# Kernel tuning notes

Measured on AMD Instinct MI355X. Metric: run time of the kernel, lower is better.

Reference implementation:

```python
import jax, jax.numpy as jnp
import numpy as np

B, N = 2048, 4095  # batch, number of spherical points (cumsum length = N+1)


def setup_inputs() -> dict:
    key = jax.random.key(0)
    k1, k2, k3, k4, k5 = jax.random.split(key, 5)
    return {
        "origin_3D": jax.random.uniform(k1, (B, 3, 1), dtype=jnp.float32),
        "spherical_3D": jax.random.uniform(k2, (B, 3, N), dtype=jnp.float32),
        "origin_2D": jax.random.uniform(k3, (B, 3, 1), dtype=jnp.float32),
        "spherical_2D": jax.random.uniform(k4, (B, 3, N), dtype=jnp.float32),
        "deformation_field": jax.random.uniform(k5, (B, 2, N), dtype=jnp.float32),
    }


def _cart(origin, spherical):
    # spherical: [B, 3, N] with rows (r, theta, phi)
    r, theta, phi = spherical[:, 0, :], spherical[:, 1, :], spherical[:, 2, :]
    st = jnp.sin(theta)
    x = r * st * jnp.cos(phi)
    y = r * st * jnp.sin(phi)
    z = r * jnp.cos(theta)
    shape = jnp.stack((x, y, z), axis=1)            # [B, 3, N]
    full = jnp.concatenate((origin, shape), axis=2)  # [B, 3, N+1]
    # torch.matmul(full, triu(ones)) == prefix sum along the last axis
    return jnp.cumsum(full, axis=2)


def reference(origin_3D, spherical_3D, origin_2D, spherical_2D, deformation_field):
    spherical_3D_deformed = spherical_3D.at[:, 1:, :].add(deformation_field)
    original_cart = _cart(origin_2D, spherical_2D)            # [B, 3, N+1]
    deformed_cart = _cart(origin_3D, spherical_3D_deformed)   # [B, 3, N+1]
    per_pt = jnp.sum(jnp.abs(deformed_cart - original_cart), axis=1)  # [B, N+1]
    return jnp.sum(jnp.mean(per_pt, axis=1))  # scalar
```

## Files before the change

### kernel.cpp

```cpp
#include <hip/hip_runtime.h>


#define BATCH 2048
#define NPTS  4095
#define POS   4096
#define T     512
#define NW    8
#define M     8
#define CH    8
#define BUFSZ 4352

__launch_bounds__(T, 6)
__global__ void mpd_loss_kernel(const float* __restrict__ origin3,
                                const float* __restrict__ sph3,
                                const float* __restrict__ origin2,
                                const float* __restrict__ sph2,
                                const float* __restrict__ def,
                                float* __restrict__ bsum) {
    __shared__ float bufx[BUFSZ];
    __shared__ float bufy[BUFSZ];
    __shared__ float bufz[BUFSZ];
    __shared__ float wtotx[NW], wtoty[NW], wtotz[NW];
    __shared__ float wsum[NW];

    const int b    = blockIdx.x;
    const int t    = threadIdx.x;
    const int lane = t & 63;
    const int w    = t >> 6;

    const float* r3  = sph3 + (size_t)b * 3 * NPTS;
    const float* th3 = r3 + NPTS;
    const float* ph3 = th3 + NPTS;
    const float* r2  = sph2 + (size_t)b * 3 * NPTS;
    const float* th2 = r2 + NPTS;
    const float* ph2 = th2 + NPTS;
    const float* d0  = def + (size_t)b * 2 * NPTS;
    const float* d1  = d0 + NPTS;

    #pragma unroll
    for (int m = 0; m < M; ++m) {
        const int j = m * T + t;
        float dx, dy, dz;
        if (m == 0 && t == 0) {
            const float* o3 = origin3 + (size_t)b * 3;
            const float* o2 = origin2 + (size_t)b * 3;
            dx = o3[0] - o2[0];
            dy = o3[1] - o2[1];
            dz = o3[2] - o2[2];
        } else {
            const int n = j - 1;
            const float R3  = r3[n];
            const float Th3 = th3[n] + d0[n];
            const float Ph3 = ph3[n] + d1[n];
            const float R2  = r2[n];
            const float Th2 = th2[n];
            const float Ph2 = ph2[n];
            float s3, c3, sp3, cp3, s2, c2, sp2, cp2;
            __sincosf(Th3, &s3, &c3);
            __sincosf(Ph3, &sp3, &cp3);
            __sincosf(Th2, &s2, &c2);
            __sincosf(Ph2, &sp2, &cp2);
            const float rs3 = R3 * s3;
            const float rs2 = R2 * s2;
            dx = rs3 * cp3 - rs2 * cp2;
            dy = rs3 * sp3 - rs2 * sp2;
            dz = R3 * c3 - R2 * c2;
        }
        const int a = j + (j >> 4);
        bufx[a] = dx;
        bufy[a] = dy;
        bufz[a] = dz;
    }
    __syncthreads();

    const int jb = t * CH;
    const int ba = jb + (jb >> 4);
    float vx[CH], vy[CH], vz[CH];
    float tx = 0.f, ty = 0.f, tz = 0.f;
    #pragma unroll
    for (int k = 0; k < CH; ++k) {
        vx[k] = bufx[ba + k]; tx += vx[k];
        vy[k] = bufy[ba + k]; ty += vy[k];
        vz[k] = bufz[ba + k]; tz += vz[k];
    }

    float ix = tx, iy = ty, iz = tz;
    #pragma unroll
    for (int off = 1; off < 64; off <<= 1) {
        const float ux = __shfl_up(ix, off, 64);
        const float uy = __shfl_up(iy, off, 64);
        const float uz = __shfl_up(iz, off, 64);
        if (lane >= off) { ix += ux; iy += uy; iz += uz; }
    }
    if (lane == 63) { wtotx[w] = ix; wtoty[w] = iy; wtotz[w] = iz; }
    __syncthreads();

    float wox = 0.f, woy = 0.f, woz = 0.f;
    #pragma unroll
    for (int ww = 0; ww < NW; ++ww) {
        if (ww < w) { wox += wtotx[ww]; woy += wtoty[ww]; woz += wtotz[ww]; }
    }

    float px = wox + (ix - tx);
    float py = woy + (iy - ty);
    float pz = woz + (iz - tz);
    float acc = 0.f;
    #pragma unroll
    for (int k = 0; k < CH; ++k) {
        px += vx[k]; py += vy[k]; pz += vz[k];
        acc += fabsf(px) + fabsf(py) + fabsf(pz);
    }

    #pragma unroll
    for (int off = 32; off > 0; off >>= 1) acc += __shfl_down(acc, off, 64);
    if (lane == 0) wsum[w] = acc;
    __syncthreads();
    if (t == 0) {
        float s = 0.f;
        #pragma unroll
        for (int i = 0; i < NW; ++i) s += wsum[i];
        bsum[b] = s * (1.0f / POS);
    }
}

__launch_bounds__(256)
__global__ void reduce_kernel(const float* __restrict__ bsum, float* __restrict__ out) {
    const int t = threadIdx.x;
    float acc = 0.f;
    #pragma unroll
    for (int i = 0; i < BATCH / 256; ++i) acc += bsum[t + i * 256];
    #pragma unroll
    for (int off = 32; off > 0; off >>= 1) acc += __shfl_down(acc, off, 64);
    __shared__ float wred[4];
    if ((t & 63) == 0) wred[t >> 6] = acc;
    __syncthreads();
    if (t == 0) out[0] = wred[0] + wred[1] + wred[2] + wred[3];
}

extern "C" void kernel_launch(void* const* d_in, const int* in_sizes, int n_in,
                              void* d_out, int out_size, void* d_ws, size_t ws_size,
                              hipStream_t stream) {
    const float* origin3 = (const float*)d_in[0];
    const float* sph3    = (const float*)d_in[1];
    const float* origin2 = (const float*)d_in[2];
    const float* sph2    = (const float*)d_in[3];
    const float* def     = (const float*)d_in[4];
    float* out  = (float*)d_out;
    float* bsum = (float*)d_ws;

    mpd_loss_kernel<<<BATCH, T, 0, stream>>>(origin3, sph3, origin2, sph2, def, bsum);
    reduce_kernel<<<1, 256, 0, stream>>>(bsum, out);
}
```

Baseline: 267.7 us.

## Load contiguous points per thread with vector loads and drop the shared-memory transpose

Each thread now reads its own contiguous block of eight points straight from global memory as two 4-wide vector loads per input row, with the last thread shifting its second load to stay in bounds. It computes the Cartesian deltas in registers and feeds them directly into the scan, so the large shared staging buffers and one barrier go away. The origin term is added to every prefix instead of being stored as element zero. The loads are unaligned and strided by 32 bytes per thread, which may coalesce less well than the old lane-contiguous reads, and the occupancy hint drops from 6 to 4 blocks.

```diff
diff --git a/kernel.cpp b/kernel.cpp
--- a/kernel.cpp
+++ b/kernel.cpp
@@ -6,27 +6,25 @@
 #define POS   4096
 #define T     512
 #define NW    8
-#define M     8
 #define CH    8
-#define BUFSZ 4352
 
-__launch_bounds__(T, 6)
+typedef float f4 __attribute__((ext_vector_type(4), aligned(4)));
+
+__launch_bounds__(T, 4)
 __global__ void mpd_loss_kernel(const float* __restrict__ origin3,
                                 const float* __restrict__ sph3,
                                 const float* __restrict__ origin2,
                                 const float* __restrict__ sph2,
                                 const float* __restrict__ def,
                                 float* __restrict__ bsum) {
-    __shared__ float bufx[BUFSZ];
-    __shared__ float bufy[BUFSZ];
-    __shared__ float bufz[BUFSZ];
-    __shared__ float wtotx[NW], wtoty[NW], wtotz[NW];
+    __shared__ float wtot[3][NW];
     __shared__ float wsum[NW];
 
     const int b    = blockIdx.x;
     const int t    = threadIdx.x;
     const int lane = t & 63;
     const int w    = t >> 6;
+    const bool lastT = (t == T - 1);
 
     const float* r3  = sph3 + (size_t)b * 3 * NPTS;
     const float* th3 = r3 + NPTS;
@@ -37,51 +35,56 @@
     const float* d0  = def + (size_t)b * 2 * NPTS;
     const float* d1  = d0 + NPTS;
 
-    #pragma unroll
-    for (int m = 0; m < M; ++m) {
-        const int j = m * T + t;
-        float dx, dy, dz;
-        if (m == 0 && t == 0) {
-            const float* o3 = origin3 + (size_t)b * 3;
-            const float* o2 = origin2 + (size_t)b * 3;
-            dx = o3[0] - o2[0];
-            dy = o3[1] - o2[1];
-            dz = o3[2] - o2[2];
-        } else {
-            const int n = j - 1;
-            const float R3  = r3[n];
-            const float Th3 = th3[n] + d0[n];
-            const float Ph3 = ph3[n] + d1[n];
-            const float R2  = r2[n];
-            const float Th2 = th2[n];
-            const float Ph2 = ph2[n];
-            float s3, c3, sp3, cp3, s2, c2, sp2, cp2;
-            __sincosf(Th3, &s3, &c3);
-            __sincosf(Ph3, &sp3, &cp3);
-            __sincosf(Th2, &s2, &c2);
-            __sincosf(Ph2, &sp2, &cp2);
-            const float rs3 = R3 * s3;
-            const float rs2 = R2 * s2;
-            dx = rs3 * cp3 - rs2 * cp2;
-            dy = rs3 * sp3 - rs2 * sp2;
-            dz = R3 * c3 - R2 * c2;
-        }
-        const int a = j + (j >> 4);
-        bufx[a] = dx;
-        bufy[a] = dy;
-        bufz[a] = dz;
-    }
-    __syncthreads();
+    const int n0 = t * CH;
+    const int n1 = lastT ? (n0 + 3) : (n0 + 4);
 
-    const int jb = t * CH;
-    const int ba = jb + (jb >> 4);
-    float vx[CH], vy[CH], vz[CH];
+    const f4 aR3 = *(const f4*)(r3  + n0);  const f4 bR3 = *(const f4*)(r3  + n1);
+    const f4 aT3 = *(const f4*)(th3 + n0);  const f4 bT3 = *(const f4*)(th3 + n1);
+    const f4 aP3 = *(const f4*)(ph3 + n0);  const f4 bP3 = *(const f4*)(ph3 + n1);
+    const f4 aR2 = *(const f4*)(r2  + n0);  const f4 bR2 = *(const f4*)(r2  + n1);
+    const f4 aT2 = *(const f4*)(th2 + n0);  const f4 bT2 = *(const f4*)(th2 + n1);
+    const f4 aP2 = *(const f4*)(ph2 + n0);  const f4 bP2 = *(const f4*)(ph2 + n1);
+    const f4 aD0 = *(const f4*)(d0  + n0);  const f4 bD0 = *(const f4*)(d0  + n1);
+    const f4 aD1 = *(const f4*)(d1  + n0);  const f4 bD1 = *(const f4*)(d1  + n1);
+
+    #define EXT(A, Bv, out)                          \
+        out[0] = A[0]; out[1] = A[1];                \
+        out[2] = A[2]; out[3] = A[3];                \
+        out[4] = lastT ? Bv[1] : Bv[0];              \
+        out[5] = lastT ? Bv[2] : Bv[1];              \
+        out[6] = lastT ? Bv[3] : Bv[2];              \
+        out[7] = Bv[3];
+
+    float eR3[8], eT3[8], eP3[8], eR2[8], eT2[8], eP2[8], eD0[8], eD1[8];
+    EXT(aR3, bR3, eR3); EXT(aT3, bT3, eT3); EXT(aP3, bP3, eP3);
+    EXT(aR2, bR2, eR2); EXT(aT2, bT2, eT2); EXT(aP2, bP2, eP2);
+    EXT(aD0, bD0, eD0); EXT(aD1, bD1, eD1);
+    #undef EXT
+
+    float dx[CH], dy[CH], dz[CH];
     float tx = 0.f, ty = 0.f, tz = 0.f;
     #pragma unroll
     for (int k = 0; k < CH; ++k) {
-        vx[k] = bufx[ba + k]; tx += vx[k];
-        vy[k] = bufy[ba + k]; ty += vy[k];
-        vz[k] = bufz[ba + k]; tz += vz[k];
+        const bool valid = (k < 7) || !lastT;
+        const float R3  = eR3[k];
+        const float Th3 = eT3[k] + eD0[k];
+        const float Ph3 = eP3[k] + eD1[k];
+        const float R2  = eR2[k];
+        const float Th2 = eT2[k];
+        const float Ph2 = eP2[k];
+        float s3, c3, sp3, cp3, s2, c2, sp2, cp2;
+        __sincosf(Th3, &s3, &c3);
+        __sincosf(Ph3, &sp3, &cp3);
+        __sincosf(Th2, &s2, &c2);
+        __sincosf(Ph2, &sp2, &cp2);
+        const float rs3 = R3 * s3;
+        const float rs2 = R2 * s2;
+        float ddx = rs3 * cp3 - rs2 * cp2;
+        float ddy = rs3 * sp3 - rs2 * sp2;
+        float ddz = R3 * c3 - R2 * c2;
+        if (!valid) { ddx = 0.f; ddy = 0.f; ddz = 0.f; }
+        dx[k] = ddx; dy[k] = ddy; dz[k] = ddz;
+        tx += ddx; ty += ddy; tz += ddz;
     }
 
     float ix = tx, iy = ty, iz = tz;
@@ -92,23 +95,30 @@
         const float uz = __shfl_up(iz, off, 64);
         if (lane >= off) { ix += ux; iy += uy; iz += uz; }
     }
-    if (lane == 63) { wtotx[w] = ix; wtoty[w] = iy; wtotz[w] = iz; }
+    if (lane == 63) { wtot[0][w] = ix; wtot[1][w] = iy; wtot[2][w] = iz; }
     __syncthreads();
 
     float wox = 0.f, woy = 0.f, woz = 0.f;
     #pragma unroll
     for (int ww = 0; ww < NW; ++ww) {
-        if (ww < w) { wox += wtotx[ww]; woy += wtoty[ww]; woz += wtotz[ww]; }
+        if (ww < w) { wox += wtot[0][ww]; woy += wtot[1][ww]; woz += wtot[2][ww]; }
     }
 
-    float px = wox + (ix - tx);
-    float py = woy + (iy - ty);
-    float pz = woz + (iz - tz);
-    float acc = 0.f;
+    const float* o3 = origin3 + (size_t)b * 3;
+    const float* o2 = origin2 + (size_t)b * 3;
+    const float odx = o3[0] - o2[0];
+    const float ody = o3[1] - o2[1];
+    const float odz = o3[2] - o2[2];
+
+    float px = odx + wox + (ix - tx);
+    float py = ody + woy + (iy - ty);
+    float pz = odz + woz + (iz - tz);
+    float acc = (t == 0) ? (fabsf(odx) + fabsf(ody) + fabsf(odz)) : 0.f;
     #pragma unroll
     for (int k = 0; k < CH; ++k) {
-        px += vx[k]; py += vy[k]; pz += vz[k];
-        acc += fabsf(px) + fabsf(py) + fabsf(pz);
+        const bool valid = (k < 7) || !lastT;
+        px += dx[k]; py += dy[k]; pz += dz[k];
+        if (valid) acc += fabsf(px) + fabsf(py) + fabsf(pz);
     }
 
     #pragma unroll
```

Measured after the change: 263.6 us. Within noise of the previous version (-1.5%).
